# Optimization experiments

Measured on AMD Instinct MI355X. Metric: run time of the kernel, lower is better.

Reference implementation:

```python
import jax, jax.numpy as jnp
import numpy as np

C = 256
INTER = 32  # C // reduction_ratio(8)
B, H, W = 4, 64, 64


def setup_inputs() -> dict:
    key = jax.random.key(0)
    ks = jax.random.split(key, 8)
    x = jax.random.normal(ks[0], (B, C, H, W), dtype=jnp.float32)
    # 1x1 conv weights stored as [out, in] matrices + biases
    Wq = jax.random.normal(ks[1], (INTER, C), dtype=jnp.float32) * (1.0 / np.sqrt(C))
    bq = jnp.zeros((INTER,), dtype=jnp.float32)
    Wk = jax.random.normal(ks[2], (INTER, C), dtype=jnp.float32) * (1.0 / np.sqrt(C))
    bk = jnp.zeros((INTER,), dtype=jnp.float32)
    Wv = jax.random.normal(ks[3], (C, C), dtype=jnp.float32) * (1.0 / np.sqrt(C))
    bv = jnp.zeros((C,), dtype=jnp.float32)
    gamma = jnp.zeros((1,), dtype=jnp.float32)
    return {"x": x, "Wq": Wq, "bq": bq, "Wk": Wk, "bk": bk, "Wv": Wv, "bv": bv, "gamma": gamma}


def reference(x, Wq, bq, Wk, bk, Wv, bv, gamma):
    b, c, h, w = x.shape
    n = h * w
    xf = x.reshape(b, c, n)  # [B,C,N]
    # 1x1 convs == channel matmuls
    q = jnp.einsum('ic,bcn->bin', Wq, xf) + bq[None, :, None]  # [B,I,N]
    k = jnp.einsum('ic,bcn->bin', Wk, xf) + bk[None, :, None]  # [B,I,N]
    v = jnp.einsum('oc,bcn->bon', Wv, xf) + bv[None, :, None]  # [B,C,N]
    scale = INTER ** (-0.5)
    attn = jnp.einsum('bin,bim->bnm', q, k) * scale  # [B,N,N]
    attn = jax.nn.softmax(attn, axis=-1)
    out = jnp.einsum('bcm,bnm->bcn', v, attn)  # value @ attn^T
    out = out.reshape(b, c, h, w)
    return gamma[0] * out + x
```

## Files before the change

### kernel.cpp

```cpp
#include <hip/hip_runtime.h>
#include <hip/hip_bf16.h>
#include <cstddef>
#include <cstdint>

#define BB 4
#define CC 256
#define II 32
#define NN 4096

#define SCALE_Q 0.25505572751402893f

typedef __attribute__((ext_vector_type(8))) short bf16x8;
typedef __attribute__((ext_vector_type(16))) float f32x16;

static __device__ __forceinline__ int cvt_pk_bf16(float lo, float hi) {
  int d;
  asm("v_cvt_pk_bf16_f32 %0, %1, %2" : "=v"(d) : "v"(lo), "v"(hi));
  return d;
}
static __device__ __forceinline__ void perm32swap_f(float& a, float& b) {
  asm("v_permlane32_swap_b32 %0, %1" : "+v"(a), "+v"(b));
}
static __device__ __forceinline__ float max3f(float a, float b, float c) {
  float d;
  asm("v_max3_f32 %0, %1, %2, %3" : "=v"(d) : "v"(a), "v"(b), "v"(c));
  return d;
}
static __device__ __forceinline__ f32x16 zero16() {
  f32x16 z;
#pragma unroll
  for (int i = 0; i < 16; ++i) z[i] = 0.0f;
  return z;
}
static __device__ __forceinline__ void mfma_bf16_first(bf16x8 a, bf16x8 b, f32x16& c) {
  asm("s_nop 1\n\tv_mfma_f32_32x32x16_bf16 %0, %1, %2, %0"
      : "+v"(c) : "v"(a), "v"(b));
}
static __device__ __forceinline__ void mfma_bf16_last(bf16x8 a, bf16x8 b, f32x16& c) {
  asm("v_mfma_f32_32x32x16_bf16 %0, %1, %2, %0\n\ts_nop 7\n\ts_nop 7"
      : "+v"(c) : "v"(a), "v"(b));
}
static __device__ __forceinline__ bf16x8 pack8(float f0, float f1, float f2,
    float f3, float f4, float f5, float f6, float f7) {
  union { int w[4]; bf16x8 v8; } u;
  u.w[0] = cvt_pk_bf16(f0, f1);
  u.w[1] = cvt_pk_bf16(f2, f3);
  u.w[2] = cvt_pk_bf16(f4, f5);
  u.w[3] = cvt_pk_bf16(f6, f7);
  return u.v8;
}
static __device__ __forceinline__ ushort f2bfu(float f) {
  union { __hip_bfloat16 h; ushort u; } cv;
  cv.h = __float2bfloat16(f);
  return cv.u;
}
static __device__ __forceinline__ int pack4_fp8(float a, float b, float c, float d) {
  int r = __builtin_amdgcn_cvt_pk_fp8_f32(a, b, 0, false);
  r = __builtin_amdgcn_cvt_pk_fp8_f32(c, d, r, true);
  return r;
}
static __device__ __forceinline__ unsigned char f2fp8(float f) {
  return (unsigned char)(__builtin_amdgcn_cvt_pk_fp8_f32(f, f, 0, false) & 0xff);
}


__global__ __launch_bounds__(64) void prepack_w(
    const float* __restrict__ Wq, const float* __restrict__ Wk,
    const float* __restrict__ Wv, ushort* __restrict__ wpre) {
  const int g = blockIdx.x;
  const int ks = blockIdx.y;
  const int lane = threadIdx.x;
  const int l31 = lane & 31;
  const int h = lane >> 5;
  const float* src = (g == 0) ? (Wq + (size_t)l31 * CC)
                   : (g == 1) ? (Wk + (size_t)l31 * CC)
                              : (Wv + (size_t)((g - 2) * 32 + l31) * CC);
  const int c = ks * 16 + h * 8;
  const float4 a = *(const float4*)(src + c);
  const float4 b = *(const float4*)(src + c + 4);
  union { ushort us[8]; int4 i4; } pk;
  pk.us[0] = f2bfu(a.x); pk.us[1] = f2bfu(a.y);
  pk.us[2] = f2bfu(a.z); pk.us[3] = f2bfu(a.w);
  pk.us[4] = f2bfu(b.x); pk.us[5] = f2bfu(b.y);
  pk.us[6] = f2bfu(b.z); pk.us[7] = f2bfu(b.w);
  *(int4*)(wpre + ((size_t)g * 16 + ks) * 512 + lane * 8) = pk.i4;
}

__global__ __launch_bounds__(320, 2) void proj_lds(
    const float* __restrict__ bq, const float* __restrict__ bk,
    const float* __restrict__ bv, const float* __restrict__ x,
    const ushort* __restrict__ wpre,
    ushort* __restrict__ qT, ushort* __restrict__ kT,
    unsigned char* __restrict__ vT8) {
  __shared__ float xs[256 * 32];

  const int tid = threadIdx.x;
  const int w = tid >> 6;
  const int lane = tid & 63;
  const int l31 = lane & 31;
  const int h = lane >> 5;
  const int b = blockIdx.x;
  const int n0 = blockIdx.y * 32;

  {
    const float* xb = x + (size_t)b * CC * NN + n0;
    for (int i = w; i < 32; i += 5) {
      const float* src = xb + (size_t)(i * 8 + (lane >> 3)) * NN + (lane & 7) * 4;
      const float4 v = *(const float4*)src;
      *(float4*)&xs[i * 256 + lane * 4] = v;
    }
  }
  __syncthreads();

  const ushort* wp0 = wpre + (size_t)((w == 0) ? 0 : (2 + (w - 1) * 2)) * 16 * 512 + lane * 8;
  const ushort* wp1 = wp0 + 16 * 512;

  f32x16 acc0 = zero16(), acc1 = zero16();
#pragma unroll 4
  for (int ks = 0; ks < 16; ++ks) {
    const int c = ks * 16 + h * 8;
    const float* xp = &xs[c * 32 + l31];
    bf16x8 xf = pack8(xp[0], xp[32], xp[64], xp[96],
                      xp[128], xp[160], xp[192], xp[224]);
    const bf16x8 wf0 = *reinterpret_cast<const bf16x8*>(wp0 + ks * 512);
    const bf16x8 wf1 = *reinterpret_cast<const bf16x8*>(wp1 + ks * 512);
    acc0 = __builtin_amdgcn_mfma_f32_32x32x16_bf16(wf0, xf, acc0, 0, 0, 0);
    acc1 = __builtin_amdgcn_mfma_f32_32x32x16_bf16(wf1, xf, acc1, 0, 0, 0);
  }

  if (w == 0) {
    ushort* qb = qT + (size_t)(b * 128 + (n0 >> 5)) * 1024;
    ushort* kb = kT + (size_t)(b * 128 + (n0 >> 5)) * 1024;
#pragma unroll
    for (int r = 0; r < 16; ++r) {
      const int i = (r & 3) + 8 * (r >> 2) + 4 * h;
      const size_t off = (size_t)(i >> 4) * 512 + ((i >> 3) & 1) * 256 + 8 * l31 + (i & 7);
      qb[off] = f2bfu((acc0[r] + bq[i]) * SCALE_Q);
      kb[off] = f2bfu(acc1[r] + bk[i]);
    }
  } else {
    const int n = n0 + l31;
    const size_t nsub = (size_t)(n >> 4) * 512 + ((size_t)((n >> 3) & 1)) * 256 + (n & 7);
    const size_t bbase = (size_t)b * (1 << 20);
#pragma unroll
    for (int r = 0; r < 16; ++r) {
      const int rp = (r & 3) + 8 * (r >> 2) + 4 * h;
      const int c0 = (w - 1) * 64 + rp;
      const int c1 = c0 + 32;
      vT8[bbase + (size_t)(c0 >> 5) * 131072 + nsub + (c0 & 31) * 8] = f2fp8(acc0[r] + bv[c0]);
      vT8[bbase + (size_t)(c1 >> 5) * 131072 + nsub + (c1 & 31) * 8] = f2fp8(acc1[r] + bv[c1]);
    }
  }
}

__global__ __launch_bounds__(512, 4) void flash_coop(
    const ushort* __restrict__ qT, const ushort* __restrict__ kT,
    const unsigned char* __restrict__ vT8, const float* __restrict__ x,
    const float* __restrict__ gamma, float* __restrict__ out) {
  __shared__ __align__(16) unsigned char pbuf[2][32 * 264];
  __shared__ float mlds[264];
  __shared__ float slds[264];

  const int tid = threadIdx.x;
  const int lane = tid & 63;
  const int w = tid >> 6;
  const int q = lane & 31;
  const int h = lane >> 5;

  const int wg = blockIdx.x;
  const int xcd = wg & 7;
  const int b = xcd >> 1;
  const int nt = ((xcd & 1) << 6) + (wg >> 3);
  const int n0 = nt * 32;

  const ushort* qb = qT + (size_t)(b * 128 + nt) * 1024 + lane * 8;
  const bf16x8 qf0 = *reinterpret_cast<const bf16x8*>(qb);
  const bf16x8 qf1 = *reinterpret_cast<const bf16x8*>(qb + 512);

  const ushort* ktb = kT + (size_t)b * 128 * 1024;
  const unsigned char* vtb = vT8 + (size_t)b * (1 << 20) + (size_t)w * 131072 + lane * 8;

  f32x16 accA = zero16(), accB = zero16();
  float m_run = -1e30f, l_run = 0.0f;
  long vregA[8], vregB[8];

  {
    const ushort* kc = ktb + (size_t)(0 * 8 + w) * 1024 + lane * 8;
    const bf16x8 kf0 = *reinterpret_cast<const bf16x8*>(kc);
    const bf16x8 kf1 = *reinterpret_cast<const bf16x8*>(kc + 512);
    f32x16 st = zero16();
    mfma_bf16_first(kf0, qf0, st);
    mfma_bf16_last(kf1, qf1, st);

#pragma unroll
    for (int kp = 0; kp < 8; ++kp) {
      vregA[kp] = *reinterpret_cast<const long*>(vtb + (2 * kp) * 512);
      vregB[kp] = *reinterpret_cast<const long*>(vtb + (2 * kp + 1) * 512);
    }

    float m0 = max3f(st[0], st[1], st[2]);
    float m1 = max3f(st[3], st[4], st[5]);
    float m2 = max3f(st[6], st[7], st[8]);
    float m3 = max3f(st[9], st[10], st[11]);
    m0 = max3f(st[12], st[13], m0);
    m1 = max3f(st[14], st[15], m1);
    float mx = max3f(m0, m1, fmaxf(m2, m3));
    float sw1 = mx, sw2 = mx;
    perm32swap_f(sw1, sw2);
    if (lane < 32) mlds[w * 33 + q] = fmaxf(sw1, sw2);
    __syncthreads();
    float tmax = mlds[q];
#pragma unroll
    for (int i = 1; i < 8; ++i) tmax = fmaxf(tmax, mlds[i * 33 + q]);
    m_run = tmax;

#pragma unroll
    for (int r = 0; r < 16; ++r) st[r] = __builtin_amdgcn_exp2f(st[r] - m_run);
    float s0 = ((st[0] + st[1]) + (st[2] + st[3])) +
               ((st[4] + st[5]) + (st[6] + st[7]));
    float s1 = ((st[8] + st[9]) + (st[10] + st[11])) +
               ((st[12] + st[13]) + (st[14] + st[15]));
    float pssum = s0 + s1;
    float pa = pssum, pb = pssum;
    perm32swap_f(pa, pb);
    if (lane < 32) slds[w * 33 + q] = pa + pb;
#pragma unroll
    for (int rg = 0; rg < 4; ++rg) {
      const int pk = pack4_fp8(st[rg * 4], st[rg * 4 + 1], st[rg * 4 + 2], st[rg * 4 + 3]);
      *reinterpret_cast<int*>(&pbuf[0][q * 264 + w * 32 + rg * 8 + h * 4]) = pk;
    }
    __syncthreads();
    float tsum = slds[q];
#pragma unroll
    for (int i = 1; i < 8; ++i) tsum += slds[i * 33 + q];
    l_run = tsum;
  }

  for (int t = 1; t < 16; ++t) {
    const int pv = t - 1;
    const int pcur = pv & 1;
    const int pnext = t & 1;

    const ushort* kc = ktb + (size_t)(t * 8 + w) * 1024 + lane * 8;
    const bf16x8 kf0 = *reinterpret_cast<const bf16x8*>(kc);
    const bf16x8 kf1 = *reinterpret_cast<const bf16x8*>(kc + 512);

    const unsigned char* pb = &pbuf[pcur][q * 264 + h * 8];
    __builtin_amdgcn_s_setprio(1);
    long pA = *reinterpret_cast<const long*>(pb);
    long pB = *reinterpret_cast<const long*>(pb + 16);
#pragma unroll
    for (int kp = 0; kp < 8; ++kp) {
      long pAn = 0, pBn = 0;
      if (kp < 7) {
        pAn = *reinterpret_cast<const long*>(pb + (2 * kp + 2) * 16);
        pBn = *reinterpret_cast<const long*>(pb + (2 * kp + 3) * 16);
      }
      accA = __builtin_amdgcn_mfma_f32_32x32x16_fp8_fp8(vregA[kp], pA, accA, 0, 0, 0);
      accB = __builtin_amdgcn_mfma_f32_32x32x16_fp8_fp8(vregB[kp], pB, accB, 0, 0, 0);
      pA = pAn; pB = pBn;
    }

    const unsigned char* vcn = vtb + (size_t)(t * 16) * 512;
#pragma unroll
    for (int kp = 0; kp < 8; ++kp) {
      vregA[kp] = *reinterpret_cast<const long*>(vcn + (2 * kp) * 512);
      vregB[kp] = *reinterpret_cast<const long*>(vcn + (2 * kp + 1) * 512);
    }

    f32x16 st = zero16();
    mfma_bf16_first(kf0, qf0, st);
    mfma_bf16_last(kf1, qf1, st);
    __builtin_amdgcn_s_setprio(0);

    float m0 = max3f(st[0], st[1], st[2]);
    float m1 = max3f(st[3], st[4], st[5]);
    float m2 = max3f(st[6], st[7], st[8]);
    float m3 = max3f(st[9], st[10], st[11]);
    m0 = max3f(st[12], st[13], m0);
    m1 = max3f(st[14], st[15], m1);
    float mx = max3f(m0, m1, fmaxf(m2, m3));
    float sw1 = mx, sw2 = mx;
    perm32swap_f(sw1, sw2);
    if (lane < 32) mlds[w * 33 + q] = fmaxf(sw1, sw2);
    __syncthreads();
    float tmax = mlds[q];
#pragma unroll
    for (int i = 1; i < 8; ++i) tmax = fmaxf(tmax, mlds[i * 33 + q]);

    if (__any(tmax > m_run + 8.0f)) {
      const float mnew = fmaxf(m_run, tmax);
      const float f = __builtin_amdgcn_exp2f(m_run - mnew);
#pragma unroll
      for (int r = 0; r < 16; ++r) { accA[r] *= f; accB[r] *= f; }
      l_run *= f;
      m_run = mnew;
    }

#pragma unroll
    for (int r = 0; r < 16; ++r) st[r] = __builtin_amdgcn_exp2f(st[r] - m_run);
    float s0 = ((st[0] + st[1]) + (st[2] + st[3])) +
               ((st[4] + st[5]) + (st[6] + st[7]));
    float s1 = ((st[8] + st[9]) + (st[10] + st[11])) +
               ((st[12] + st[13]) + (st[14] + st[15]));
    float pssum = s0 + s1;
    float pa = pssum, pb2 = pssum;
    perm32swap_f(pa, pb2);
    if (lane < 32) slds[w * 33 + q] = pa + pb2;

#pragma unroll
    for (int rg = 0; rg < 4; ++rg) {
      const int pk = pack4_fp8(st[rg * 4], st[rg * 4 + 1], st[rg * 4 + 2], st[rg * 4 + 3]);
      *reinterpret_cast<int*>(&pbuf[pnext][q * 264 + w * 32 + rg * 8 + h * 4]) = pk;
    }
    __syncthreads();

    float tsum = slds[q];
#pragma unroll
    for (int i = 1; i < 8; ++i) tsum += slds[i * 33 + q];
    l_run += tsum;
  }

  {
    const unsigned char* pb = &pbuf[1][q * 264 + h * 8];
    __builtin_amdgcn_s_setprio(1);
#pragma unroll
    for (int kp = 0; kp < 8; ++kp) {
      const long pA = *reinterpret_cast<const long*>(pb + (2 * kp) * 16);
      const long pB = *reinterpret_cast<const long*>(pb + (2 * kp + 1) * 16);
      accA = __builtin_amdgcn_mfma_f32_32x32x16_fp8_fp8(vregA[kp], pA, accA, 0, 0, 0);
      accB = __builtin_amdgcn_mfma_f32_32x32x16_fp8_fp8(vregB[kp], pB, accB, 0, 0, 0);
    }
    __builtin_amdgcn_s_setprio(0);
  }

  const float g = gamma[0];
  const float linv = 1.0f / l_run;
#pragma unroll
  for (int r = 0; r < 16; ++r) {
    const int c = w * 32 + (r & 3) + 8 * (r >> 2) + 4 * h;
    const size_t idx = ((size_t)b * CC + c) * NN + n0 + q;
    out[idx] = g * (accA[r] + accB[r]) * linv + x[idx];
  }
}

extern "C" void kernel_launch(void* const* d_in, const int* in_sizes, int n_in,
                              void* d_out, int out_size, void* d_ws, size_t ws_size,
                              hipStream_t stream) {
  const float* x = (const float*)d_in[0];
  const float* Wq = (const float*)d_in[1];
  const float* bq = (const float*)d_in[2];
  const float* Wk = (const float*)d_in[3];
  const float* bk = (const float*)d_in[4];
  const float* Wv = (const float*)d_in[5];
  const float* bv = (const float*)d_in[6];
  const float* gamma = (const float*)d_in[7];
  float* out = (float*)d_out;

  ushort* qT = (ushort*)d_ws;
  ushort* kT = qT + (size_t)BB * 128 * 1024;
  unsigned char* vT8 = (unsigned char*)(kT + (size_t)BB * 128 * 1024);
  ushort* wpre = (ushort*)(vT8 + (size_t)BB * (1 << 20));

  prepack_w<<<dim3(10, 16), dim3(64), 0, stream>>>(Wq, Wk, Wv, wpre);
  proj_lds<<<dim3(BB, NN / 32), dim3(320), 0, stream>>>(
      bq, bk, bv, x, wpre, qT, kT, vT8);
  flash_coop<<<dim3(512), dim3(512), 0, stream>>>(
      qT, kT, vT8, x, gamma, out);
}
```

Before: 64.96 us.

## Split flash attention block into producer and consumer wave groups

Restructures the cooperative flash kernel so that four waves act as producers, computing QK scores, softmax statistics and the FP8 probability tile, while the other four waves consume it and run the PV MFMAs. The rescale factors and the final row sums pass through LDS. The goal is to overlap the softmax/score phase with the PV matmul in separate waves instead of running them serially in every wave. In exchange, each consumer wave now owns two full channel groups, and V is streamed from global memory inside the loop instead of being prefetched into registers. The heavier per-wave work, the new LDS handoffs and the uneven load between the two groups may offset the overlap.

```diff
diff --git a/kernel.cpp b/kernel.cpp
--- a/kernel.cpp
+++ b/kernel.cpp
@@ -153,19 +153,23 @@
   }
 }
 
-__global__ __launch_bounds__(512, 4) void flash_coop(
+__global__ __launch_bounds__(512, 4) void flash_pc(
     const ushort* __restrict__ qT, const ushort* __restrict__ kT,
     const unsigned char* __restrict__ vT8, const float* __restrict__ x,
     const float* __restrict__ gamma, float* __restrict__ out) {
   __shared__ __align__(16) unsigned char pbuf[2][32 * 264];
-  __shared__ float mlds[264];
-  __shared__ float slds[264];
+  __shared__ float mlds[144];
+  __shared__ float slds[144];
+  __shared__ float fbuf[2][32];
+  __shared__ float lbuf[32];
 
   const int tid = threadIdx.x;
   const int lane = tid & 63;
   const int w = tid >> 6;
   const int q = lane & 31;
   const int h = lane >> 5;
+  const bool prod = (w < 4);
+  const int p = w & 3;
 
   const int wg = blockIdx.x;
   const int xcd = wg & 7;
@@ -173,174 +177,214 @@
   const int nt = ((xcd & 1) << 6) + (wg >> 3);
   const int n0 = nt * 32;
 
-  const ushort* qb = qT + (size_t)(b * 128 + nt) * 1024 + lane * 8;
-  const bf16x8 qf0 = *reinterpret_cast<const bf16x8*>(qb);
-  const bf16x8 qf1 = *reinterpret_cast<const bf16x8*>(qb + 512);
-
   const ushort* ktb = kT + (size_t)b * 128 * 1024;
-  const unsigned char* vtb = vT8 + (size_t)b * (1 << 20) + (size_t)w * 131072 + lane * 8;
+
+  bf16x8 qf0 = {}, qf1 = {};
+  bf16x8 kA0 = {}, kA1 = {}, kB0 = {}, kB1 = {};
+  float m_run = -1e30f, l_run = 0.0f;
+  if (prod) {
+    const ushort* qb = qT + (size_t)(b * 128 + nt) * 1024 + lane * 8;
+    qf0 = *reinterpret_cast<const bf16x8*>(qb);
+    qf1 = *reinterpret_cast<const bf16x8*>(qb + 512);
+    const ushort* kc = ktb + (size_t)(p * 2) * 1024 + lane * 8;
+    kA0 = *reinterpret_cast<const bf16x8*>(kc);
+    kA1 = *reinterpret_cast<const bf16x8*>(kc + 512);
+    kB0 = *reinterpret_cast<const bf16x8*>(kc + 1024);
+    kB1 = *reinterpret_cast<const bf16x8*>(kc + 1536);
+  }
 
   f32x16 accA = zero16(), accB = zero16();
-  float m_run = -1e30f, l_run = 0.0f;
-  long vregA[8], vregB[8];
-
-  {
-    const ushort* kc = ktb + (size_t)(0 * 8 + w) * 1024 + lane * 8;
-    const bf16x8 kf0 = *reinterpret_cast<const bf16x8*>(kc);
-    const bf16x8 kf1 = *reinterpret_cast<const bf16x8*>(kc + 512);
-    f32x16 st = zero16();
-    mfma_bf16_first(kf0, qf0, st);
-    mfma_bf16_last(kf1, qf1, st);
-
-#pragma unroll
-    for (int kp = 0; kp < 8; ++kp) {
-      vregA[kp] = *reinterpret_cast<const long*>(vtb + (2 * kp) * 512);
-      vregB[kp] = *reinterpret_cast<const long*>(vtb + (2 * kp + 1) * 512);
-    }
-
-    float m0 = max3f(st[0], st[1], st[2]);
-    float m1 = max3f(st[3], st[4], st[5]);
-    float m2 = max3f(st[6], st[7], st[8]);
-    float m3 = max3f(st[9], st[10], st[11]);
-    m0 = max3f(st[12], st[13], m0);
-    m1 = max3f(st[14], st[15], m1);
-    float mx = max3f(m0, m1, fmaxf(m2, m3));
+  const unsigned char* vtbA = vT8 + ((size_t)b << 20) + (size_t)(2 * p) * 131072 + lane * 8;
+  const unsigned char* vtbB = vtbA + 131072;
+  if (!prod) __builtin_amdgcn_s_setprio(1);
+
+  if (prod) {
+    f32x16 st0 = zero16(), st1 = zero16();
+    mfma_bf16_first(kA0, qf0, st0);
+    mfma_bf16_first(kB0, qf0, st1);
+    mfma_bf16_last(kA1, qf1, st0);
+    mfma_bf16_last(kB1, qf1, st1);
+    const ushort* kn = ktb + (size_t)(8 + p * 2) * 1024 + lane * 8;
+    kA0 = *reinterpret_cast<const bf16x8*>(kn);
+    kA1 = *reinterpret_cast<const bf16x8*>(kn + 512);
+    kB0 = *reinterpret_cast<const bf16x8*>(kn + 1024);
+    kB1 = *reinterpret_cast<const bf16x8*>(kn + 1536);
+    float a0 = max3f(st0[0], st0[1], st0[2]);
+    float a1 = max3f(st0[3], st0[4], st0[5]);
+    float a2 = max3f(st0[6], st0[7], st0[8]);
+    float a3 = max3f(st0[9], st0[10], st0[11]);
+    a0 = max3f(st0[12], st0[13], a0);
+    a1 = max3f(st0[14], st0[15], a1);
+    a2 = max3f(st1[0], st1[1], a2);
+    a3 = max3f(st1[2], st1[3], a3);
+    a0 = max3f(st1[4], st1[5], a0);
+    a1 = max3f(st1[6], st1[7], a1);
+    a2 = max3f(st1[8], st1[9], a2);
+    a3 = max3f(st1[10], st1[11], a3);
+    a0 = max3f(st1[12], st1[13], a0);
+    a1 = max3f(st1[14], st1[15], a1);
+    float mx = max3f(a0, a1, fmaxf(a2, a3));
     float sw1 = mx, sw2 = mx;
     perm32swap_f(sw1, sw2);
-    if (lane < 32) mlds[w * 33 + q] = fmaxf(sw1, sw2);
+    if (lane < 32) mlds[p * 33 + q] = fmaxf(sw1, sw2);
     __syncthreads();
-    float tmax = mlds[q];
-#pragma unroll
-    for (int i = 1; i < 8; ++i) tmax = fmaxf(tmax, mlds[i * 33 + q]);
+    float tmax = fmaxf(fmaxf(mlds[q], mlds[33 + q]),
+                       fmaxf(mlds[66 + q], mlds[99 + q]));
     m_run = tmax;
-
-#pragma unroll
-    for (int r = 0; r < 16; ++r) st[r] = __builtin_amdgcn_exp2f(st[r] - m_run);
-    float s0 = ((st[0] + st[1]) + (st[2] + st[3])) +
-               ((st[4] + st[5]) + (st[6] + st[7]));
-    float s1 = ((st[8] + st[9]) + (st[10] + st[11])) +
-               ((st[12] + st[13]) + (st[14] + st[15]));
-    float pssum = s0 + s1;
-    float pa = pssum, pb = pssum;
-    perm32swap_f(pa, pb);
-    if (lane < 32) slds[w * 33 + q] = pa + pb;
+#pragma unroll
+    for (int r = 0; r < 16; ++r) st0[r] = __builtin_amdgcn_exp2f(st0[r] - m_run);
+#pragma unroll
+    for (int r = 0; r < 16; ++r) st1[r] = __builtin_amdgcn_exp2f(st1[r] - m_run);
+    float s0 = ((st0[0] + st0[1]) + (st0[2] + st0[3])) +
+               ((st0[4] + st0[5]) + (st0[6] + st0[7])) +
+               ((st0[8] + st0[9]) + (st0[10] + st0[11])) +
+               ((st0[12] + st0[13]) + (st0[14] + st0[15]));
+    float s1 = ((st1[0] + st1[1]) + (st1[2] + st1[3])) +
+               ((st1[4] + st1[5]) + (st1[6] + st1[7])) +
+               ((st1[8] + st1[9]) + (st1[10] + st1[11])) +
+               ((st1[12] + st1[13]) + (st1[14] + st1[15]));
+    float ps = s0 + s1, pa = ps, pb2 = ps;
+    perm32swap_f(pa, pb2);
+    if (lane < 32) slds[p * 33 + q] = pa + pb2;
 #pragma unroll
     for (int rg = 0; rg < 4; ++rg) {
-      const int pk = pack4_fp8(st[rg * 4], st[rg * 4 + 1], st[rg * 4 + 2], st[rg * 4 + 3]);
-      *reinterpret_cast<int*>(&pbuf[0][q * 264 + w * 32 + rg * 8 + h * 4]) = pk;
-    }
+      const int pk0 = pack4_fp8(st0[rg * 4], st0[rg * 4 + 1], st0[rg * 4 + 2], st0[rg * 4 + 3]);
+      *reinterpret_cast<int*>(&pbuf[0][q * 264 + p * 64 + rg * 8 + h * 4]) = pk0;
+      const int pk1 = pack4_fp8(st1[rg * 4], st1[rg * 4 + 1], st1[rg * 4 + 2], st1[rg * 4 + 3]);
+      *reinterpret_cast<int*>(&pbuf[0][q * 264 + p * 64 + 32 + rg * 8 + h * 4]) = pk1;
+    }
+    if (p == 0 && lane < 32) fbuf[0][q] = 1.0f;
     __syncthreads();
-    float tsum = slds[q];
-#pragma unroll
-    for (int i = 1; i < 8; ++i) tsum += slds[i * 33 + q];
-    l_run = tsum;
+    l_run = slds[q] + slds[33 + q] + slds[66 + q] + slds[99 + q];
+  } else {
+    __syncthreads();
+    __syncthreads();
   }
 
   for (int t = 1; t < 16; ++t) {
-    const int pv = t - 1;
-    const int pcur = pv & 1;
-    const int pnext = t & 1;
-
-    const ushort* kc = ktb + (size_t)(t * 8 + w) * 1024 + lane * 8;
-    const bf16x8 kf0 = *reinterpret_cast<const bf16x8*>(kc);
-    const bf16x8 kf1 = *reinterpret_cast<const bf16x8*>(kc + 512);
-
-    const unsigned char* pb = &pbuf[pcur][q * 264 + h * 8];
-    __builtin_amdgcn_s_setprio(1);
-    long pA = *reinterpret_cast<const long*>(pb);
-    long pB = *reinterpret_cast<const long*>(pb + 16);
-#pragma unroll
-    for (int kp = 0; kp < 8; ++kp) {
-      long pAn = 0, pBn = 0;
-      if (kp < 7) {
-        pAn = *reinterpret_cast<const long*>(pb + (2 * kp + 2) * 16);
-        pBn = *reinterpret_cast<const long*>(pb + (2 * kp + 3) * 16);
+    if (!prod) {
+      const int slot = (t - 1) & 1;
+      const float f = fbuf[slot][q];
+      if (__any(f != 1.0f)) {
+#pragma unroll
+        for (int r = 0; r < 16; ++r) { accA[r] *= f; accB[r] *= f; }
       }
-      accA = __builtin_amdgcn_mfma_f32_32x32x16_fp8_fp8(vregA[kp], pA, accA, 0, 0, 0);
-      accB = __builtin_amdgcn_mfma_f32_32x32x16_fp8_fp8(vregB[kp], pB, accB, 0, 0, 0);
-      pA = pAn; pB = pBn;
-    }
-
-    const unsigned char* vcn = vtb + (size_t)(t * 16) * 512;
-#pragma unroll
-    for (int kp = 0; kp < 8; ++kp) {
-      vregA[kp] = *reinterpret_cast<const long*>(vcn + (2 * kp) * 512);
-      vregB[kp] = *reinterpret_cast<const long*>(vcn + (2 * kp + 1) * 512);
-    }
-
-    f32x16 st = zero16();
-    mfma_bf16_first(kf0, qf0, st);
-    mfma_bf16_last(kf1, qf1, st);
-    __builtin_amdgcn_s_setprio(0);
-
-    float m0 = max3f(st[0], st[1], st[2]);
-    float m1 = max3f(st[3], st[4], st[5]);
-    float m2 = max3f(st[6], st[7], st[8]);
-    float m3 = max3f(st[9], st[10], st[11]);
-    m0 = max3f(st[12], st[13], m0);
-    m1 = max3f(st[14], st[15], m1);
-    float mx = max3f(m0, m1, fmaxf(m2, m3));
-    float sw1 = mx, sw2 = mx;
-    perm32swap_f(sw1, sw2);
-    if (lane < 32) mlds[w * 33 + q] = fmaxf(sw1, sw2);
-    __syncthreads();
-    float tmax = mlds[q];
-#pragma unroll
-    for (int i = 1; i < 8; ++i) tmax = fmaxf(tmax, mlds[i * 33 + q]);
-
-    if (__any(tmax > m_run + 8.0f)) {
-      const float mnew = fmaxf(m_run, tmax);
-      const float f = __builtin_amdgcn_exp2f(m_run - mnew);
+      const unsigned char* pb = &pbuf[slot][q * 264 + h * 8];
+      const unsigned char* vA = vtbA + (size_t)((t - 1) * 16) * 512;
+      const unsigned char* vB = vtbB + (size_t)((t - 1) * 16) * 512;
+#pragma unroll
+      for (int kt = 0; kt < 16; ++kt) {
+        const long pf = *reinterpret_cast<const long*>(pb + kt * 16);
+        const long va = *reinterpret_cast<const long*>(vA + kt * 512);
+        accA = __builtin_amdgcn_mfma_f32_32x32x16_fp8_fp8(va, pf, accA, 0, 0, 0);
+        const long vb = *reinterpret_cast<const long*>(vB + kt * 512);
+        accB = __builtin_amdgcn_mfma_f32_32x32x16_fp8_fp8(vb, pf, accB, 0, 0, 0);
+      }
+      __syncthreads();
+      __syncthreads();
+    } else {
+      f32x16 st0 = zero16(), st1 = zero16();
+      mfma_bf16_first(kA0, qf0, st0);
+      mfma_bf16_first(kB0, qf0, st1);
+      mfma_bf16_last(kA1, qf1, st0);
+      mfma_bf16_last(kB1, qf1, st1);
+      if (t < 15) {
+        const ushort* kn = ktb + (size_t)((t + 1) * 8 + p * 2) * 1024 + lane * 8;
+        kA0 = *reinterpret_cast<const bf16x8*>(kn);
+        kA1 = *reinterpret_cast<const bf16x8*>(kn + 512);
+        kB0 = *reinterpret_cast<const bf16x8*>(kn + 1024);
+        kB1 = *reinterpret_cast<const bf16x8*>(kn + 1536);
+      }
+      float a0 = max3f(st0[0], st0[1], st0[2]);
+      float a1 = max3f(st0[3], st0[4], st0[5]);
+      float a2 = max3f(st0[6], st0[7], st0[8]);
+      float a3 = max3f(st0[9], st0[10], st0[11]);
+      a0 = max3f(st0[12], st0[13], a0);
+      a1 = max3f(st0[14], st0[15], a1);
+      a2 = max3f(st1[0], st1[1], a2);
+      a3 = max3f(st1[2], st1[3], a3);
+      a0 = max3f(st1[4], st1[5], a0);
+      a1 = max3f(st1[6], st1[7], a1);
+      a2 = max3f(st1[8], st1[9], a2);
+      a3 = max3f(st1[10], st1[11], a3);
+      a0 = max3f(st1[12], st1[13], a0);
+      a1 = max3f(st1[14], st1[15], a1);
+      float mx = max3f(a0, a1, fmaxf(a2, a3));
+      float sw1 = mx, sw2 = mx;
+      perm32swap_f(sw1, sw2);
+      if (lane < 32) mlds[p * 33 + q] = fmaxf(sw1, sw2);
+      __syncthreads();
+      float tmax = fmaxf(fmaxf(mlds[q], mlds[33 + q]),
+                         fmaxf(mlds[66 + q], mlds[99 + q]));
+      float f = 1.0f;
+      if (__any(tmax > m_run + 8.0f)) {
+        const float mnew = fmaxf(m_run, tmax);
+        f = __builtin_amdgcn_exp2f(m_run - mnew);
+        l_run *= f;
+        m_run = mnew;
+      }
+      if (p == 0 && lane < 32) fbuf[t & 1][q] = f;
+#pragma unroll
+      for (int r = 0; r < 16; ++r) st0[r] = __builtin_amdgcn_exp2f(st0[r] - m_run);
+#pragma unroll
+      for (int r = 0; r < 16; ++r) st1[r] = __builtin_amdgcn_exp2f(st1[r] - m_run);
+      float s0 = ((st0[0] + st0[1]) + (st0[2] + st0[3])) +
+                 ((st0[4] + st0[5]) + (st0[6] + st0[7])) +
+                 ((st0[8] + st0[9]) + (st0[10] + st0[11])) +
+                 ((st0[12] + st0[13]) + (st0[14] + st0[15]));
+      float s1 = ((st1[0] + st1[1]) + (st1[2] + st1[3])) +
+                 ((st1[4] + st1[5]) + (st1[6] + st1[7])) +
+                 ((st1[8] + st1[9]) + (st1[10] + st1[11])) +
+                 ((st1[12] + st1[13]) + (st1[14] + st1[15]));
+      float ps = s0 + s1, pa = ps, pb2 = ps;
+      perm32swap_f(pa, pb2);
+      if (lane < 32) slds[p * 33 + q] = pa + pb2;
+#pragma unroll
+      for (int rg = 0; rg < 4; ++rg) {
+        const int pk0 = pack4_fp8(st0[rg * 4], st0[rg * 4 + 1], st0[rg * 4 + 2], st0[rg * 4 + 3]);
+        *reinterpret_cast<int*>(&pbuf[t & 1][q * 264 + p * 64 + rg * 8 + h * 4]) = pk0;
+        const int pk1 = pack4_fp8(st1[rg * 4], st1[rg * 4 + 1], st1[rg * 4 + 2], st1[rg * 4 + 3]);
+        *reinterpret_cast<int*>(&pbuf[t & 1][q * 264 + p * 64 + 32 + rg * 8 + h * 4]) = pk1;
+      }
+      __syncthreads();
+      l_run += slds[q] + slds[33 + q] + slds[66 + q] + slds[99 + q];
+    }
+  }
+
+  if (!prod) {
+    const float f = fbuf[1][q];
+    if (__any(f != 1.0f)) {
 #pragma unroll
       for (int r = 0; r < 16; ++r) { accA[r] *= f; accB[r] *= f; }
-      l_run *= f;
-      m_run = mnew;
-    }
-
-#pragma unroll
-    for (int r = 0; r < 16; ++r) st[r] = __builtin_amdgcn_exp2f(st[r] - m_run);
-    float s0 = ((st[0] + st[1]) + (st[2] + st[3])) +
-               ((st[4] + st[5]) + (st[6] + st[7]));
-    float s1 = ((st[8] + st[9]) + (st[10] + st[11])) +
-               ((st[12] + st[13]) + (st[14] + st[15]));
-    float pssum = s0 + s1;
-    float pa = pssum, pb2 = pssum;
-    perm32swap_f(pa, pb2);
-    if (lane < 32) slds[w * 33 + q] = pa + pb2;
-
-#pragma unroll
-    for (int rg = 0; rg < 4; ++rg) {
-      const int pk = pack4_fp8(st[rg * 4], st[rg * 4 + 1], st[rg * 4 + 2], st[rg * 4 + 3]);
-      *reinterpret_cast<int*>(&pbuf[pnext][q * 264 + w * 32 + rg * 8 + h * 4]) = pk;
-    }
-    __syncthreads();
-
-    float tsum = slds[q];
-#pragma unroll
-    for (int i = 1; i < 8; ++i) tsum += slds[i * 33 + q];
-    l_run += tsum;
-  }
-
-  {
+    }
     const unsigned char* pb = &pbuf[1][q * 264 + h * 8];
-    __builtin_amdgcn_s_setprio(1);
-#pragma unroll
-    for (int kp = 0; kp < 8; ++kp) {
-      const long pA = *reinterpret_cast<const long*>(pb + (2 * kp) * 16);
-      const long pB = *reinterpret_cast<const long*>(pb + (2 * kp + 1) * 16);
-      accA = __builtin_amdgcn_mfma_f32_32x32x16_fp8_fp8(vregA[kp], pA, accA, 0, 0, 0);
-      accB = __builtin_amdgcn_mfma_f32_32x32x16_fp8_fp8(vregB[kp], pB, accB, 0, 0, 0);
-    }
-    __builtin_amdgcn_s_setprio(0);
-  }
-
-  const float g = gamma[0];
-  const float linv = 1.0f / l_run;
-#pragma unroll
-  for (int r = 0; r < 16; ++r) {
-    const int c = w * 32 + (r & 3) + 8 * (r >> 2) + 4 * h;
-    const size_t idx = ((size_t)b * CC + c) * NN + n0 + q;
-    out[idx] = g * (accA[r] + accB[r]) * linv + x[idx];
+    const unsigned char* vA = vtbA + (size_t)(15 * 16) * 512;
+    const unsigned char* vB = vtbB + (size_t)(15 * 16) * 512;
+#pragma unroll
+    for (int kt = 0; kt < 16; ++kt) {
+      const long pf = *reinterpret_cast<const long*>(pb + kt * 16);
+      const long va = *reinterpret_cast<const long*>(vA + kt * 512);
+      accA = __builtin_amdgcn_mfma_f32_32x32x16_fp8_fp8(va, pf, accA, 0, 0, 0);
+      const long vb = *reinterpret_cast<const long*>(vB + kt * 512);
+      accB = __builtin_amdgcn_mfma_f32_32x32x16_fp8_fp8(vb, pf, accB, 0, 0, 0);
+    }
+  } else {
+    if (p == 0 && lane < 32) lbuf[q] = l_run;
+  }
+  __syncthreads();
+
+  if (!prod) {
+    const float g = gamma[0];
+    const float linv = 1.0f / lbuf[q];
+#pragma unroll
+    for (int r = 0; r < 16; ++r) {
+      const int rp = (r & 3) + 8 * (r >> 2) + 4 * h;
+      const int c0 = p * 64 + rp;
+      const size_t i0 = ((size_t)b * CC + c0) * NN + n0 + q;
+      const size_t i1 = ((size_t)b * CC + c0 + 32) * NN + n0 + q;
+      out[i0] = g * accA[r] * linv + x[i0];
+      out[i1] = g * accB[r] * linv + x[i1];
+    }
   }
 }
 
@@ -365,6 +409,6 @@
   prepack_w<<<dim3(10, 16), dim3(64), 0, stream>>>(Wq, Wk, Wv, wpre);
   proj_lds<<<dim3(BB, NN / 32), dim3(320), 0, stream>>>(
       bq, bk, bv, x, wpre, qT, kT, vT8);
-  flash_coop<<<dim3(512), dim3(512), 0, stream>>>(
+  flash_pc<<<dim3(512), dim3(512), 0, stream>>>(
       qT, kT, vT8, x, gamma, out);
 }
```

Result: slower. 67.67 us (+4.2%).
